# Kernel optimization log

Measured on AMD Instinct MI355X. Metric: run time of the kernel, lower is better.

## Reference

```python
import jax, jax.numpy as jnp
import numpy as np

# static config (matches init_kwargs)
T = 4            # number of block shape types
N_PER = 512      # blocks per type (sorted by type)
BLOCK_DIM = 32
OBST_DIM = 16
TGT_DIM = 16
HID = 128
HEADS = 4
ROUNDS = 3
N_OBS = 1024
N_TGT = 1023
GROUND_ACT = 8
BLOCK_ACT = 4 * 2  # n_receiving_faces * num_block_actions_per_face


def setup_inputs() -> dict:
    key = jax.random.key(0)
    ks = jax.random.split(key, 32)

    def rnd(i, shape, fan_in=None):
        s = 1.0 if fan_in is None else 1.0 / np.sqrt(fan_in)
        return (jax.random.normal(ks[i], shape, jnp.float32) * s).astype(jnp.float32)

    blocks_feat = rnd(0, (T * N_PER, BLOCK_DIM))
    type_col = jnp.repeat(jnp.arange(T), N_PER).astype(jnp.float32)[:, None]
    blocks = jnp.concatenate([blocks_feat, type_col], axis=1)  # [2048, 33]
    obstacles = rnd(1, (N_OBS, OBST_DIM))
    targets = rnd(2, (N_TGT, TGT_DIM))

    return dict(
        blocks=blocks, obstacles=obstacles, targets=targets,
        # per-type block encoders (stacked)
        Wb1=rnd(3, (T, BLOCK_DIM, HID), BLOCK_DIM), bb1=jnp.zeros((T, HID), jnp.float32),
        Wb2=rnd(4, (T, HID, HID), HID), bb2=jnp.zeros((T, HID), jnp.float32),
        # per-type block decoders (stacked)
        Wd=rnd(5, (T, 2 * HID, BLOCK_ACT), 2 * HID), bd=jnp.zeros((T, BLOCK_ACT), jnp.float32),
        # obstacle encoder
        Wo1=rnd(6, (OBST_DIM, HID), OBST_DIM), bo1=jnp.zeros((HID,), jnp.float32),
        Wo2=rnd(7, (HID, HID), HID), bo2=jnp.zeros((HID,), jnp.float32),
        # target encoder
        Wt1=rnd(8, (TGT_DIM, HID), TGT_DIM), bt1=jnp.zeros((HID,), jnp.float32),
        Wt2=rnd(9, (HID, HID), HID), bt2=jnp.zeros((HID,), jnp.float32),
        # ground param
        ground_param=(2.0 * jax.random.uniform(ks[10], (HID,), jnp.float32) - 1.0),
        # attention layer
        Wk=rnd(11, (HEADS, HID, HID), HID), Wq=rnd(12, (HEADS, HID, HID), HID),
        Wv=rnd(13, (HEADS, HID, HID), HID), Wm=jnp.ones((HEADS,), jnp.float32),
        Wg=rnd(14, (HID, HID), HID), bg=jnp.zeros((HID,), jnp.float32),
        # global + ground decoders
        Wglob=rnd(15, (HID, HID), HID), bglob=jnp.zeros((HID,), jnp.float32),
        Wgr=rnd(16, (2 * HID, GROUND_ACT), 2 * HID), bgr=jnp.zeros((GROUND_ACT,), jnp.float32),
    )


def _mlp2(x, W1, b1, W2, b2):
    return jax.nn.relu(x @ W1 + b1) @ W2 + b2


def reference(blocks, obstacles, targets, Wb1, bb1, Wb2, bb2, Wd, bd,
              Wo1, bo1, Wo2, bo2, Wt1, bt1, Wt2, bt2, ground_param,
              Wk, Wq, Wv, Wm, Wg, bg, Wglob, bglob, Wgr, bgr):
    # per-type block encoding (blocks sorted by type, equal counts -> static reshape)
    bf = blocks[:, :BLOCK_DIM].reshape(T, N_PER, BLOCK_DIM)
    h = jax.nn.relu(jnp.einsum('tnd,tdh->tnh', bf, Wb1) + bb1[:, None, :])
    xb = (jnp.einsum('tnh,thk->tnk', h, Wb2) + bb2[:, None, :]).reshape(T * N_PER, HID)
    xo = _mlp2(obstacles, Wo1, bo1, Wo2, bo2)
    xt = _mlp2(targets, Wt1, bt1, Wt2, bt2)
    x = jnp.concatenate([ground_param[None, :], xb, xo, xt], axis=0)  # [N, HID]

    for _ in range(ROUNDS):
        k = jnp.einsum('nd,hde->hne', x, Wk)
        q = jnp.einsum('nd,hde->hne', x, Wq)
        v = jnp.einsum('nd,hde->hne', x, Wv)
        e = jnp.einsum('hne,hme->hnm', q, k)           # [H, N, N]
        att = jax.nn.softmax(e, axis=-1)
        out = jnp.einsum('h,hnm,hme->ne', Wm, att, v)  # head-weighted sum
        x = x + jax.nn.relu((x + out) @ Wg + bg)

    G = x.mean(axis=0) @ Wglob + bglob                 # [HID]
    q_ground = jnp.concatenate([x[0], G]) @ Wgr + bgr  # [GROUND_ACT]

    xb2 = x[1:1 + T * N_PER].reshape(T, N_PER, HID)
    feat = jnp.concatenate([xb2, jnp.broadcast_to(G, (T, N_PER, HID))], axis=-1)
    q_blocks = jnp.einsum('tnf,tfa->tna', feat, Wd) + bd[:, None, :]  # [T, N_PER, 8]
    return q_ground, q_blocks
```

## Files before the change

kernel.cpp:

```cpp
#include <hip/hip_runtime.h>

#define HID 128
#define NNODES 4096
#define T 4
#define N_PER 512

typedef unsigned short u16;
typedef __attribute__((ext_vector_type(8))) short bf16x8;
typedef __attribute__((ext_vector_type(4))) float f32x4;

#define MFMA(a, b, c) __builtin_amdgcn_mfma_f32_16x16x32_bf16((a), (b), (c), 0, 0, 0)

__device__ __forceinline__ u16 bfhi(float f) {
  union { float f; unsigned u; } v; v.f = f;
  return (u16)(v.u >> 16);
}
__device__ __forceinline__ float bff(u16 h) {
  union { float f; unsigned u; } v; v.u = ((unsigned)h) << 16;
  return v.f;
}

__global__ __launch_bounds__(128) void encode_kernel(
    const float* __restrict__ blocks, const float* __restrict__ obstacles,
    const float* __restrict__ targets,
    const float* __restrict__ Wb1, const float* __restrict__ bb1,
    const float* __restrict__ Wb2, const float* __restrict__ bb2,
    const float* __restrict__ Wo1, const float* __restrict__ bo1,
    const float* __restrict__ Wo2, const float* __restrict__ bo2,
    const float* __restrict__ Wt1, const float* __restrict__ bt1,
    const float* __restrict__ Wt2, const float* __restrict__ bt2,
    const float* __restrict__ ground, float* __restrict__ x) {
  int n = blockIdx.x;
  int j = threadIdx.x;
  __shared__ float in_s[32];
  __shared__ float h_s[128];
  if (n == 0) {
    x[j] = ground[j];
    return;
  }
  const float *W1, *b1, *W2, *b2, *inp;
  int D;
  if (n <= 2048) {
    int b = n - 1;
    int t = b >> 9;
    inp = blocks + (size_t)b * 33;
    D = 32;
    W1 = Wb1 + (size_t)t * 32 * HID;
    b1 = bb1 + (size_t)t * HID;
    W2 = Wb2 + (size_t)t * HID * HID;
    b2 = bb2 + (size_t)t * HID;
  } else if (n <= 3072) {
    int o = n - 2049;
    inp = obstacles + (size_t)o * 16;
    D = 16;
    W1 = Wo1; b1 = bo1; W2 = Wo2; b2 = bo2;
  } else {
    int tg = n - 3073;
    inp = targets + (size_t)tg * 16;
    D = 16;
    W1 = Wt1; b1 = bt1; W2 = Wt2; b2 = bt2;
  }
  if (j < D) in_s[j] = inp[j];
  __syncthreads();
  float acc = b1[j];
  for (int d = 0; d < D; d++) acc += in_s[d] * W1[d * HID + j];
  h_s[j] = fmaxf(acc, 0.f);
  __syncthreads();
  float acc2 = b2[j];
  for (int k = 0; k < HID; k++) acc2 += h_s[k] * W2[k * HID + j];
  x[(size_t)n * HID + j] = acc2;
}

__global__ __launch_bounds__(256) void qkv_kernel(
    const float* __restrict__ x, const float* __restrict__ Wk,
    const float* __restrict__ Wq, const float* __restrict__ Wv,
    u16* __restrict__ khi, u16* __restrict__ klo,
    u16* __restrict__ qhi, u16* __restrict__ qlo,
    u16* __restrict__ vthi, u16* __restrict__ vtlo) {
  int m = blockIdx.x;
  int h = m & 3;
  int sel = m >> 2;
  const float* W = (sel == 0 ? Wk : (sel == 1 ? Wq : Wv)) + (size_t)h * HID * HID;
  int r0 = blockIdx.y * 32;
  __shared__ float xs[32][132];
  int t = threadIdx.x;
  for (int i = t; i < 32 * 32; i += 256) {
    int r = i >> 5, c = (i & 31) * 4;
    *(float4*)&xs[r][c] = *(const float4*)(x + (size_t)(r0 + r) * HID + c);
  }
  __syncthreads();
  int j = t & 127;
  int rh = t >> 7;
  float acc[16];
#pragma unroll
  for (int i = 0; i < 16; i++) acc[i] = 0.f;
  for (int d = 0; d < HID; d += 4) {
    float w0 = W[(d + 0) * HID + j];
    float w1 = W[(d + 1) * HID + j];
    float w2 = W[(d + 2) * HID + j];
    float w3 = W[(d + 3) * HID + j];
#pragma unroll
    for (int i = 0; i < 16; i++) {
      float4 xv = *(const float4*)&xs[rh * 16 + i][d];
      acc[i] = fmaf(xv.x, w0, fmaf(xv.y, w1, fmaf(xv.z, w2, fmaf(xv.w, w3, acc[i]))));
    }
  }
  if (sel == 2) {
    __align__(16) u16 hb[16], lb[16];
#pragma unroll
    for (int i = 0; i < 16; i++) {
      float v = acc[i];
      u16 hi = bfhi(v);
      hb[i] = hi;
      lb[i] = bfhi(v - bff(hi));
    }
    u16* dh = vthi + ((size_t)(h * HID + j)) * NNODES + r0 + rh * 16;
    u16* dl = vtlo + ((size_t)(h * HID + j)) * NNODES + r0 + rh * 16;
    *(bf16x8*)dh = *(const bf16x8*)hb;
    *(bf16x8*)(dh + 8) = *(const bf16x8*)(hb + 8);
    *(bf16x8*)dl = *(const bf16x8*)lb;
    *(bf16x8*)(dl + 8) = *(const bf16x8*)(lb + 8);
  } else {
    u16* oh = (sel == 0 ? khi : qhi);
    u16* ol = (sel == 0 ? klo : qlo);
#pragma unroll
    for (int i = 0; i < 16; i++) {
      int row = r0 + rh * 16 + i;
      float v = acc[i];
      u16 hi = bfhi(v);
      oh[((size_t)h * NNODES + row) * HID + j] = hi;
      ol[((size_t)h * NNODES + row) * HID + j] = bfhi(v - bff(hi));
    }
  }
}

__global__ __launch_bounds__(256) void attn_kernel(
    const u16* __restrict__ qhi, const u16* __restrict__ qlo,
    const u16* __restrict__ khi, const u16* __restrict__ klo,
    const u16* __restrict__ vthi, const u16* __restrict__ vtlo,
    float* __restrict__ outh) {
  int h = blockIdx.x;
  int q0 = blockIdx.y * 64;
  __shared__ __align__(16) u16 Kls[2][32 * 136];
  __shared__ __align__(16) u16 Vls[2][128 * 40];
  __shared__ __align__(16) u16 Pls[4][2][16 * 40];
  int t = threadIdx.x;
  int w = t >> 6;
  int l = t & 63;
  int lr = l & 15;
  int lg = l >> 4;

  int qrow = q0 + w * 16 + lr;
  const u16* qbh = qhi + ((size_t)h * NNODES + qrow) * HID + lg * 8;
  const u16* qbl = qlo + ((size_t)h * NNODES + qrow) * HID + lg * 8;
  bf16x8 qfh[4], qfl[4];
#pragma unroll
  for (int c = 0; c < 4; c++) {
    qfh[c] = *(const bf16x8*)(qbh + c * 32);
    qfl[c] = *(const bf16x8*)(qbl + c * 32);
  }

  f32x4 out[8];
#pragma unroll
  for (int i = 0; i < 8; i++) out[i] = (f32x4){0.f, 0.f, 0.f, 0.f};
  float run_m[4], run_l[4];
#pragma unroll
  for (int r = 0; r < 4; r++) { run_m[r] = -1e30f; run_l[r] = 0.f; }

  const u16* kbh = khi + (size_t)h * NNODES * HID;
  const u16* kbl = klo + (size_t)h * NNODES * HID;
  const u16* vbh = vthi + (size_t)h * HID * NNODES;
  const u16* vbl = vtlo + (size_t)h * HID * NNODES;

  for (int kt = 0; kt < NNODES / 32; kt++) {
#pragma unroll
    for (int i = 0; i < 2; i++) {
      int flat = i * 256 + t;
      int node = flat >> 4, ch = flat & 15;
      *(bf16x8*)&Kls[0][node * 136 + ch * 8] =
          *(const bf16x8*)(kbh + ((size_t)(kt * 32 + node)) * HID + ch * 8);
      *(bf16x8*)&Kls[1][node * 136 + ch * 8] =
          *(const bf16x8*)(kbl + ((size_t)(kt * 32 + node)) * HID + ch * 8);
      int d = flat >> 2, c2 = flat & 3;
      *(bf16x8*)&Vls[0][d * 40 + c2 * 8] =
          *(const bf16x8*)(vbh + (size_t)d * NNODES + kt * 32 + c2 * 8);
      *(bf16x8*)&Vls[1][d * 40 + c2 * 8] =
          *(const bf16x8*)(vbl + (size_t)d * NNODES + kt * 32 + c2 * 8);
    }
    __syncthreads();

    f32x4 ehh[2], ehl[2], elh[2];
#pragma unroll
    for (int ti = 0; ti < 2; ti++) {
      ehh[ti] = (f32x4){0.f, 0.f, 0.f, 0.f};
      ehl[ti] = (f32x4){0.f, 0.f, 0.f, 0.f};
      elh[ti] = (f32x4){0.f, 0.f, 0.f, 0.f};
    }
#pragma unroll
    for (int c = 0; c < 4; c++) {
#pragma unroll
      for (int ti = 0; ti < 2; ti++) {
        bf16x8 bh = *(const bf16x8*)&Kls[0][(ti * 16 + lr) * 136 + c * 32 + lg * 8];
        bf16x8 bl = *(const bf16x8*)&Kls[1][(ti * 16 + lr) * 136 + c * 32 + lg * 8];
        ehh[ti] = MFMA(qfh[c], bh, ehh[ti]);
        ehl[ti] = MFMA(qfh[c], bl, ehl[ti]);
        elh[ti] = MFMA(qfl[c], bh, elh[ti]);
      }
    }
    f32x4 e0 = ehh[0] + ehl[0] + elh[0];
    f32x4 e1 = ehh[1] + ehl[1] + elh[1];

    float sc[4];
#pragma unroll
    for (int r = 0; r < 4; r++) {
      float m2 = fmaxf(e0[r], e1[r]);
      m2 = fmaxf(m2, __shfl_xor(m2, 1));
      m2 = fmaxf(m2, __shfl_xor(m2, 2));
      m2 = fmaxf(m2, __shfl_xor(m2, 4));
      m2 = fmaxf(m2, __shfl_xor(m2, 8));
      float nm = fmaxf(run_m[r], m2);
      sc[r] = __expf(run_m[r] - nm);
      run_m[r] = nm;
      float p0 = __expf(e0[r] - nm);
      float p1 = __expf(e1[r] - nm);
      float lt = p0 + p1;
      lt += __shfl_xor(lt, 1);
      lt += __shfl_xor(lt, 2);
      lt += __shfl_xor(lt, 4);
      lt += __shfl_xor(lt, 8);
      run_l[r] = run_l[r] * sc[r] + lt;
      int prow = 4 * lg + r;
      u16 p0h = bfhi(p0);
      u16 p1h = bfhi(p1);
      Pls[w][0][prow * 40 + lr] = p0h;
      Pls[w][0][prow * 40 + 16 + lr] = p1h;
      Pls[w][1][prow * 40 + lr] = bfhi(p0 - bff(p0h));
      Pls[w][1][prow * 40 + 16 + lr] = bfhi(p1 - bff(p1h));
    }
#pragma unroll
    for (int dt = 0; dt < 8; dt++) {
      out[dt][0] *= sc[0];
      out[dt][1] *= sc[1];
      out[dt][2] *= sc[2];
      out[dt][3] *= sc[3];
    }

    bf16x8 ah = *(const bf16x8*)&Pls[w][0][lr * 40 + lg * 8];
    bf16x8 al = *(const bf16x8*)&Pls[w][1][lr * 40 + lg * 8];
#pragma unroll
    for (int dt = 0; dt < 8; dt++) {
      bf16x8 bh = *(const bf16x8*)&Vls[0][(dt * 16 + lr) * 40 + lg * 8];
      bf16x8 bl = *(const bf16x8*)&Vls[1][(dt * 16 + lr) * 40 + lg * 8];
      out[dt] = MFMA(ah, bh, out[dt]);
      out[dt] = MFMA(ah, bl, out[dt]);
      out[dt] = MFMA(al, bh, out[dt]);
    }
    __syncthreads();
  }

  float inv[4];
#pragma unroll
  for (int r = 0; r < 4; r++) inv[r] = 1.f / run_l[r];
  float* ob = outh + ((size_t)h * NNODES + q0 + w * 16) * HID;
#pragma unroll
  for (int dt = 0; dt < 8; dt++)
#pragma unroll
    for (int r = 0; r < 4; r++)
      ob[(size_t)(4 * lg + r) * HID + dt * 16 + lr] = out[dt][r] * inv[r];
}

__global__ __launch_bounds__(256) void gate_kernel(
    float* __restrict__ x, const float* __restrict__ outh,
    const float* __restrict__ Wm, const float* __restrict__ Wg,
    const float* __restrict__ bg) {
  int r0 = blockIdx.x * 32;
  __shared__ float ss[32][132];
  int t = threadIdx.x;
  float wm0 = Wm[0], wm1 = Wm[1], wm2 = Wm[2], wm3 = Wm[3];
  for (int i = t; i < 32 * 32; i += 256) {
    int r = i >> 5, c = (i & 31) * 4;
    size_t off = (size_t)(r0 + r) * HID + c;
    float4 xv = *(const float4*)(x + off);
    float4 o0 = *(const float4*)(outh + 0ul * NNODES * HID + off);
    float4 o1 = *(const float4*)(outh + 1ul * NNODES * HID + off);
    float4 o2 = *(const float4*)(outh + 2ul * NNODES * HID + off);
    float4 o3 = *(const float4*)(outh + 3ul * NNODES * HID + off);
    float4 s;
    s.x = xv.x + wm0 * o0.x + wm1 * o1.x + wm2 * o2.x + wm3 * o3.x;
    s.y = xv.y + wm0 * o0.y + wm1 * o1.y + wm2 * o2.y + wm3 * o3.y;
    s.z = xv.z + wm0 * o0.z + wm1 * o1.z + wm2 * o2.z + wm3 * o3.z;
    s.w = xv.w + wm0 * o0.w + wm1 * o1.w + wm2 * o2.w + wm3 * o3.w;
    *(float4*)&ss[r][c] = s;
  }
  __syncthreads();
  int j = t & 127;
  int rh = t >> 7;
  float acc[16];
#pragma unroll
  for (int i = 0; i < 16; i++) acc[i] = bg[j];
  for (int d = 0; d < HID; d += 4) {
    float w0 = Wg[(d + 0) * HID + j];
    float w1 = Wg[(d + 1) * HID + j];
    float w2 = Wg[(d + 2) * HID + j];
    float w3 = Wg[(d + 3) * HID + j];
#pragma unroll
    for (int i = 0; i < 16; i++) {
      float4 sv = *(const float4*)&ss[rh * 16 + i][d];
      acc[i] = fmaf(sv.x, w0, fmaf(sv.y, w1, fmaf(sv.z, w2, fmaf(sv.w, w3, acc[i]))));
    }
  }
#pragma unroll
  for (int i = 0; i < 16; i++) {
    size_t r = (size_t)(r0 + rh * 16 + i) * HID + j;
    x[r] = x[r] + fmaxf(acc[i], 0.f);
  }
}

__global__ __launch_bounds__(128) void colsum_kernel(const float* __restrict__ x,
                                                     float* __restrict__ xsum) {
  int j = threadIdx.x;
  int r0 = blockIdx.x * 32;
  float s = 0.f;
  for (int r = 0; r < 32; r++) s += x[(size_t)(r0 + r) * HID + j];
  atomicAdd(&xsum[j], s);
}

__global__ __launch_bounds__(128) void ground_kernel(
    const float* __restrict__ x, const float* __restrict__ xsum,
    const float* __restrict__ Wglob, const float* __restrict__ bglob,
    const float* __restrict__ Wgr, const float* __restrict__ bgr,
    float* __restrict__ G, float* __restrict__ dout) {
  __shared__ float xm[128];
  __shared__ float Gs[128];
  int j = threadIdx.x;
  xm[j] = xsum[j] * (1.f / 4096.f);
  __syncthreads();
  float acc = bglob[j];
  for (int d = 0; d < 128; d++) acc += xm[d] * Wglob[d * 128 + j];
  G[j] = acc;
  Gs[j] = acc;
  __syncthreads();
  if (j < 8) {
    float a = bgr[j];
    for (int d = 0; d < 128; d++) a += x[d] * Wgr[d * 8 + j];
    for (int d = 0; d < 128; d++) a += Gs[d] * Wgr[(128 + d) * 8 + j];
    dout[j] = a;
  }
}

__global__ __launch_bounds__(256) void qblocks_kernel(
    const float* __restrict__ x, const float* __restrict__ G,
    const float* __restrict__ Wd, const float* __restrict__ bd,
    float* __restrict__ dout) {
  int r0 = blockIdx.x * 32;
  int tt = r0 >> 9;
  __shared__ float xs[32][132];
  __shared__ float Gs[128];
  int t = threadIdx.x;
  if (t < 128) Gs[t] = G[t];
  for (int i = t; i < 32 * 32; i += 256) {
    int r = i >> 5, c = (i & 31) * 4;
    *(float4*)&xs[r][c] = *(const float4*)(x + (size_t)(1 + r0 + r) * HID + c);
  }
  __syncthreads();
  int r = t >> 3, a = t & 7;
  const float* Wt = Wd + (size_t)tt * 256 * 8;
  float acc = bd[tt * 8 + a];
  for (int d = 0; d < 128; d++) acc += xs[r][d] * Wt[d * 8 + a];
  for (int d = 0; d < 128; d++) acc += Gs[d] * Wt[(128 + d) * 8 + a];
  dout[8 + (size_t)(r0 + r) * 8 + a] = acc;
}

extern "C" void kernel_launch(void* const* d_in, const int* in_sizes, int n_in,
                              void* d_out, int out_size, void* d_ws, size_t ws_size,
                              hipStream_t stream) {
  const float* blocks    = (const float*)d_in[0];
  const float* obstacles = (const float*)d_in[1];
  const float* targets   = (const float*)d_in[2];
  const float* Wb1 = (const float*)d_in[3];
  const float* bb1 = (const float*)d_in[4];
  const float* Wb2 = (const float*)d_in[5];
  const float* bb2 = (const float*)d_in[6];
  const float* Wd  = (const float*)d_in[7];
  const float* bd  = (const float*)d_in[8];
  const float* Wo1 = (const float*)d_in[9];
  const float* bo1 = (const float*)d_in[10];
  const float* Wo2 = (const float*)d_in[11];
  const float* bo2 = (const float*)d_in[12];
  const float* Wt1 = (const float*)d_in[13];
  const float* bt1 = (const float*)d_in[14];
  const float* Wt2 = (const float*)d_in[15];
  const float* bt2 = (const float*)d_in[16];
  const float* ground = (const float*)d_in[17];
  const float* Wk = (const float*)d_in[18];
  const float* Wq = (const float*)d_in[19];
  const float* Wv = (const float*)d_in[20];
  const float* Wm = (const float*)d_in[21];
  const float* Wg = (const float*)d_in[22];
  const float* bg = (const float*)d_in[23];
  const float* Wglob = (const float*)d_in[24];
  const float* bglob = (const float*)d_in[25];
  const float* Wgr = (const float*)d_in[26];
  const float* bgr = (const float*)d_in[27];

  float* ws = (float*)d_ws;
  float* x    = ws;
  float* outh = x + 524288;
  float* xsum = outh + 2097152;
  float* G    = xsum + 128;
  u16* qhi  = (u16*)(G + 128);
  u16* qlo  = qhi + 2097152;
  u16* khi  = qlo + 2097152;
  u16* klo  = khi + 2097152;
  u16* vthi = klo + 2097152;
  u16* vtlo = vthi + 2097152;
  float* dout = (float*)d_out;

  encode_kernel<<<NNODES, 128, 0, stream>>>(
      blocks, obstacles, targets, Wb1, bb1, Wb2, bb2, Wo1, bo1, Wo2, bo2,
      Wt1, bt1, Wt2, bt2, ground, x);

  for (int round = 0; round < 3; round++) {
    qkv_kernel<<<dim3(12, NNODES / 32), 256, 0, stream>>>(
        x, Wk, Wq, Wv, khi, klo, qhi, qlo, vthi, vtlo);
    attn_kernel<<<dim3(4, NNODES / 64), 256, 0, stream>>>(
        qhi, qlo, khi, klo, vthi, vtlo, outh);
    gate_kernel<<<NNODES / 32, 256, 0, stream>>>(x, outh, Wm, Wg, bg);
  }

  hipMemsetAsync(xsum, 0, 128 * sizeof(float), stream);
  colsum_kernel<<<NNODES / 32, 128, 0, stream>>>(x, xsum);
  ground_kernel<<<1, 128, 0, stream>>>(x, xsum, Wglob, bglob, Wgr, bgr, G, dout);
  qblocks_kernel<<<64, 256, 0, stream>>>(x, G, Wd, bd, dout);
}
```

Measured before the change: 1.046 ms.

## Split attention over key range and merge partial softmax results in gate kernel

The attention kernel now splits the 4096 keys into three chunks along a new grid dimension. Each block writes unnormalized partial outputs plus its running max and sum. The gate kernel merges the splits with log-sum-exp rescaling and folds in the head weights. This triples the number of attention blocks to fill the GPU better, at the cost of extra global memory traffic for the partial outputs and a larger workspace.

```diff
diff --git a/kernel.cpp b/kernel.cpp
--- a/kernel.cpp
+++ b/kernel.cpp
@@ -4,6 +4,7 @@
 #define NNODES 4096
 #define T 4
 #define N_PER 512
+#define NSPLIT 3
 
 typedef unsigned short u16;
 typedef __attribute__((ext_vector_type(8))) short bf16x8;
@@ -138,9 +139,12 @@
     const u16* __restrict__ qhi, const u16* __restrict__ qlo,
     const u16* __restrict__ khi, const u16* __restrict__ klo,
     const u16* __restrict__ vthi, const u16* __restrict__ vtlo,
-    float* __restrict__ outh) {
+    float* __restrict__ U, float* __restrict__ ml) {
   int h = blockIdx.x;
   int q0 = blockIdx.y * 64;
+  int sp = blockIdx.z;
+  int ktb = sp * 43;
+  int kte = (sp == NSPLIT - 1) ? (NNODES / 32) : (ktb + 43);
   __shared__ __align__(16) u16 Kls[2][32 * 136];
   __shared__ __align__(16) u16 Vls[2][128 * 40];
   __shared__ __align__(16) u16 Pls[4][2][16 * 40];
@@ -172,7 +176,7 @@
   const u16* vbh = vthi + (size_t)h * HID * NNODES;
   const u16* vbl = vtlo + (size_t)h * HID * NNODES;
 
-  for (int kt = 0; kt < NNODES / 32; kt++) {
+  for (int kt = ktb; kt < kte; kt++) {
 #pragma unroll
     for (int i = 0; i < 2; i++) {
       int flat = i * 256 + t;
@@ -258,38 +262,66 @@
     __syncthreads();
   }
 
-  float inv[4];
-#pragma unroll
-  for (int r = 0; r < 4; r++) inv[r] = 1.f / run_l[r];
-  float* ob = outh + ((size_t)h * NNODES + q0 + w * 16) * HID;
+  float* ob = U + (((size_t)(sp * 4 + h) * NNODES) + q0 + w * 16) * HID;
 #pragma unroll
   for (int dt = 0; dt < 8; dt++)
 #pragma unroll
     for (int r = 0; r < 4; r++)
-      ob[(size_t)(4 * lg + r) * HID + dt * 16 + lr] = out[dt][r] * inv[r];
+      ob[(size_t)(4 * lg + r) * HID + dt * 16 + lr] = out[dt][r];
+  if (lr == 0) {
+#pragma unroll
+    for (int r = 0; r < 4; r++) {
+      size_t mi = (((size_t)(sp * 4 + h) * NNODES) + q0 + w * 16 + 4 * lg + r) * 2;
+      ml[mi] = run_m[r];
+      ml[mi + 1] = run_l[r];
+    }
+  }
 }
 
 __global__ __launch_bounds__(256) void gate_kernel(
-    float* __restrict__ x, const float* __restrict__ outh,
+    float* __restrict__ x, const float* __restrict__ U,
+    const float* __restrict__ ml,
     const float* __restrict__ Wm, const float* __restrict__ Wg,
     const float* __restrict__ bg) {
   int r0 = blockIdx.x * 32;
   __shared__ float ss[32][132];
+  __shared__ float cs[32][4][NSPLIT];
   int t = threadIdx.x;
-  float wm0 = Wm[0], wm1 = Wm[1], wm2 = Wm[2], wm3 = Wm[3];
+  if (t < 128) {
+    int r = t >> 2, h = t & 3;
+    int row = r0 + r;
+    float ms[NSPLIT], ls[NSPLIT];
+#pragma unroll
+    for (int s = 0; s < NSPLIT; s++) {
+      size_t mi = (((size_t)(s * 4 + h) * NNODES) + row) * 2;
+      ms[s] = ml[mi];
+      ls[s] = ml[mi + 1];
+    }
+    float M = fmaxf(fmaxf(ms[0], ms[1]), ms[2]);
+    float w0 = __expf(ms[0] - M), w1 = __expf(ms[1] - M), w2 = __expf(ms[2] - M);
+    float denom = ls[0] * w0 + ls[1] * w1 + ls[2] * w2;
+    float wmh = Wm[h] / denom;
+    cs[r][h][0] = w0 * wmh;
+    cs[r][h][1] = w1 * wmh;
+    cs[r][h][2] = w2 * wmh;
+  }
+  __syncthreads();
   for (int i = t; i < 32 * 32; i += 256) {
     int r = i >> 5, c = (i & 31) * 4;
     size_t off = (size_t)(r0 + r) * HID + c;
-    float4 xv = *(const float4*)(x + off);
-    float4 o0 = *(const float4*)(outh + 0ul * NNODES * HID + off);
-    float4 o1 = *(const float4*)(outh + 1ul * NNODES * HID + off);
-    float4 o2 = *(const float4*)(outh + 2ul * NNODES * HID + off);
-    float4 o3 = *(const float4*)(outh + 3ul * NNODES * HID + off);
-    float4 s;
-    s.x = xv.x + wm0 * o0.x + wm1 * o1.x + wm2 * o2.x + wm3 * o3.x;
-    s.y = xv.y + wm0 * o0.y + wm1 * o1.y + wm2 * o2.y + wm3 * o3.y;
-    s.z = xv.z + wm0 * o0.z + wm1 * o1.z + wm2 * o2.z + wm3 * o3.z;
-    s.w = xv.w + wm0 * o0.w + wm1 * o1.w + wm2 * o2.w + wm3 * o3.w;
+    float4 s = *(const float4*)(x + off);
+#pragma unroll
+    for (int h = 0; h < 4; h++) {
+#pragma unroll
+      for (int sp = 0; sp < NSPLIT; sp++) {
+        float cc = cs[r][h][sp];
+        float4 u = *(const float4*)(U + (size_t)(sp * 4 + h) * NNODES * HID + off);
+        s.x = fmaf(cc, u.x, s.x);
+        s.y = fmaf(cc, u.y, s.y);
+        s.z = fmaf(cc, u.z, s.z);
+        s.w = fmaf(cc, u.w, s.w);
+      }
+    }
     *(float4*)&ss[r][c] = s;
   }
   __syncthreads();
@@ -405,8 +437,9 @@
 
   float* ws = (float*)d_ws;
   float* x    = ws;
-  float* outh = x + 524288;
-  float* xsum = outh + 2097152;
+  float* U    = x + 524288;
+  float* ml   = U + (size_t)NSPLIT * 4 * NNODES * HID;
+  float* xsum = ml + (size_t)NSPLIT * 4 * NNODES * 2;
   float* G    = xsum + 128;
   u16* qhi  = (u16*)(G + 128);
   u16* qlo  = qhi + 2097152;
@@ -423,9 +456,9 @@
   for (int round = 0; round < 3; round++) {
     qkv_kernel<<<dim3(12, NNODES / 32), 256, 0, stream>>>(
         x, Wk, Wq, Wv, khi, klo, qhi, qlo, vthi, vtlo);
-    attn_kernel<<<dim3(4, NNODES / 64), 256, 0, stream>>>(
-        qhi, qlo, khi, klo, vthi, vtlo, outh);
-    gate_kernel<<<NNODES / 32, 256, 0, stream>>>(x, outh, Wm, Wg, bg);
+    attn_kernel<<<dim3(4, NNODES / 64, NSPLIT), 256, 0, stream>>>(
+        qhi, qlo, khi, klo, vthi, vtlo, U, ml);
+    gate_kernel<<<NNODES / 32, 256, 0, stream>>>(x, U, ml, Wm, Wg, bg);
   }
 
   hipMemsetAsync(xsum, 0, 128 * sizeof(float), stream);
```

Result: faster. 867.8 us (-17.0%).
